# Optimization experiments

Hardware: AMD Instinct MI355X
Metric: run time of the kernel (lower is better)

## Reference

```python
import jax, jax.numpy as jnp
import numpy as np

N, H, F = 131072, 256, 4096
MIN_FRAG = 3
LN_EPS = 1e-5
NORM_EPS = 1e-12
CONSISTENCY_FACTOR = 0.03
INTERMOLECULAR_WEIGHT = 0.2
SCALING_FACTOR = 0.05  # initial_strength at epoch 0 (progressive schedule, eval mode)


def _normalize(x):
    # torch F.normalize(p=2, dim=1): x / max(||x||, eps)
    n = jnp.linalg.norm(x, axis=-1, keepdims=True)
    return x / jnp.maximum(n, NORM_EPS)


def _frag_consistency(feat, frag_ids, valid):
    # size-weighted sum of per-fragment mean deviations == mean deviation over valid atoms
    m = valid.astype(feat.dtype)[:, None]
    seg_sum = jax.ops.segment_sum(feat * m, frag_ids, num_segments=F)
    seg_cnt = jax.ops.segment_sum(m, frag_ids, num_segments=F)
    means = seg_sum / jnp.maximum(seg_cnt, 1.0)  # scatter-mean over valid atoms
    sim = jnp.sum(_normalize(feat) * _normalize(means)[frag_ids], axis=-1)  # [N]
    dev = (1.0 - sim) * valid.astype(feat.dtype)
    return jnp.sum(dev) / jnp.maximum(jnp.sum(valid.astype(feat.dtype)), 1.0)


def setup_inputs() -> dict:
    key = jax.random.key(0)
    ks = jax.random.split(key, 8)
    return {
        "scalar_short": jax.random.normal(ks[0], (N, H), jnp.float32),
        "scalar_long": jax.random.normal(ks[1], (N, H), jnp.float32),
        "vector_short": jax.random.normal(ks[2], (N, 3, H), jnp.float32),
        "vector_long": jax.random.normal(ks[3], (N, 3, H), jnp.float32),
        "fragment_ids": jax.random.randint(ks[4], (N,), 0, F, dtype=jnp.int32),
        "ln_gamma": jnp.ones((H,), jnp.float32),
        "ln_beta": jnp.zeros((H,), jnp.float32),
        "W1": jax.random.normal(ks[5], (H, H), jnp.float32) / np.sqrt(H),
        "b1": jnp.zeros((H,), jnp.float32),
        "Wv": jax.random.normal(ks[6], (H, H), jnp.float32) / np.sqrt(H),
    }


def reference(scalar_short, scalar_long, vector_short, vector_long, fragment_ids,
              ln_gamma, ln_beta, W1, b1, Wv):
    # valid_mask: atoms belonging to fragments of size >= MIN_FRAG
    sizes = jax.ops.segment_sum(jnp.ones((N,), jnp.float32), fragment_ids, num_segments=F)
    valid = sizes[fragment_ids] >= MIN_FRAG  # [N] bool

    # scalar_projector: LayerNorm -> Linear -> SiLU (dropout identity at eval)
    mu = jnp.mean(scalar_short, axis=-1, keepdims=True)
    var = jnp.var(scalar_short, axis=-1, keepdims=True)
    xh = (scalar_short - mu) / jnp.sqrt(var + LN_EPS) * ln_gamma + ln_beta
    scalar_features = jax.nn.silu(xh @ W1.T + b1)  # [N, H]

    intra = _frag_consistency(scalar_features, fragment_ids, valid)

    # vector branch: per-atom magnitude = mean over 3 spatial comps of ||.||_2 over hidden
    vec_mag = jnp.mean(jnp.linalg.norm(vector_short, axis=2), axis=1, keepdims=True)  # [N,1]
    # Linear(bias=False) on mag.expand(-1,H) then [:, :1] == silu(mag * sum(Wv[0,:]))
    w0 = jnp.sum(Wv[0])
    vector_features = jax.nn.silu(vec_mag * w0)  # [N,1]
    vec_loss = _frag_consistency(vector_features, fragment_ids, valid)

    # interfragment differentiation over ALL atoms (no valid mask)
    cnt = jax.ops.segment_sum(jnp.ones((N, 1), jnp.float32), fragment_ids, num_segments=F)
    sfrag = jax.ops.segment_sum(scalar_features, fragment_ids, num_segments=F) / jnp.maximum(cnt, 1.0)
    vfrag = jax.ops.segment_sum(vec_mag, fragment_ids, num_segments=F) / jnp.maximum(cnt, 1.0)
    combined = _normalize(jnp.concatenate([sfrag, vfrag], axis=1))  # [F, H+1]
    sim = combined @ combined.T  # [F, F]
    off_sum = jnp.sum(sim) - jnp.trace(sim)
    inter = off_sum / (F * F - F + 1e-6)

    total = intra + vec_loss + INTERMOLECULAR_WEIGHT * inter
    return CONSISTENCY_FACTOR * total * SCALING_FACTOR
```

## Files before the change

### kernel.cpp

```cpp
#include <hip/hip_runtime.h>
#include <hip/hip_bf16.h>
#include <stdint.h>

#define NA 131072
#define HD 256
#define NF 4096
#define MINFRAG 3
#define LN_EPS 1e-5f
#define NEPS 1e-12f

#define OFF_CNT    0ull
#define OFF_VSUM   16384ull
#define OFF_VFSUM  32768ull
#define OFF_NVSUM  49152ull
#define OFF_FILL   65536ull
#define OFF_DBL    81920ull
#define OFF_SSUM   86016ull
#define OFF_NSUM   4280320ull
#define ZERO_BYTES 8474624ull
#define OFF_OFFS   8474624ull
#define OFF_SVEC   8491008ull
#define OFF_C0     8492032ull
#define OFF_W0     8493056ull
#define OFF_GBF    8493568ull
#define OFF_ORDER  8624640ull

#define IDX_TRACE 257
#define IDX_DEVS  258
#define IDX_DEVV  259
#define IDX_VCNT  260

typedef __attribute__((ext_vector_type(8))) short short8;
typedef __attribute__((ext_vector_type(4))) float f32x4;
union F4S8 { float4 f; short8 s; };
union BFU { __hip_bfloat16 b; unsigned short u; };

__device__ __forceinline__ unsigned short f2b(float x) {
    BFU t; t.b = __float2bfloat16(x); return t.u;
}
__device__ __forceinline__ float b2f(unsigned short u) {
    return __uint_as_float(((uint32_t)u) << 16);
}
__device__ __forceinline__ float silu_f(float x) { return x / (1.f + expf(-x)); }

__global__ __launch_bounds__(256) void k_prep(
    const float* __restrict__ W1, const float* __restrict__ gamma,
    const float* __restrict__ beta, const float* __restrict__ b1,
    const float* __restrict__ Wv,
    unsigned short* __restrict__ Gbf, float* __restrict__ svec,
    float* __restrict__ c0, float* __restrict__ w0) {
    __shared__ float red[8];
    int o = blockIdx.x;
    int t = threadIdx.x;
    if (o < HD) {
        float w = W1[(size_t)o * HD + t];
        unsigned short gb = f2b(w * gamma[t]);
        Gbf[(size_t)o * HD + t] = gb;
        float sp = b2f(gb);
        float cp = w * beta[t];
#pragma unroll
        for (int m = 32; m; m >>= 1) { sp += __shfl_xor(sp, m, 64); cp += __shfl_xor(cp, m, 64); }
        int wv = t >> 6;
        if ((t & 63) == 0) { red[wv] = sp; red[4 + wv] = cp; }
        __syncthreads();
        if (t == 0) {
            svec[o] = red[0] + red[1] + red[2] + red[3];
            c0[o]   = red[4] + red[5] + red[6] + red[7] + b1[o];
        }
    } else {
        float v = Wv[t];
#pragma unroll
        for (int m = 32; m; m >>= 1) v += __shfl_xor(v, m, 64);
        int wv = t >> 6;
        if ((t & 63) == 0) red[wv] = v;
        __syncthreads();
        if (t == 0) w0[0] = red[0] + red[1] + red[2] + red[3];
    }
}

__global__ __launch_bounds__(256) void k_stats(
    const float* __restrict__ vs, const int* __restrict__ fid,
    const float* __restrict__ w0p,
    int* __restrict__ cnt, float* __restrict__ vsum,
    float* __restrict__ vfsum, float* __restrict__ nvsum) {
    int gwave = (blockIdx.x * blockDim.x + threadIdx.x) >> 6;
    int lane = threadIdx.x & 63;
    int nw = (gridDim.x * blockDim.x) >> 6;
    float w0 = w0p[0];
    for (int i = gwave; i < NA; i += nw) {
        const float* base = vs + (size_t)i * 3 * HD;
        float4 v0 = ((const float4*)(base))[lane];
        float4 v1 = ((const float4*)(base + HD))[lane];
        float4 v2 = ((const float4*)(base + 2 * HD))[lane];
        float q0 = v0.x * v0.x + v0.y * v0.y + v0.z * v0.z + v0.w * v0.w;
        float q1 = v1.x * v1.x + v1.y * v1.y + v1.z * v1.z + v1.w * v1.w;
        float q2 = v2.x * v2.x + v2.y * v2.y + v2.z * v2.z + v2.w * v2.w;
#pragma unroll
        for (int m = 32; m; m >>= 1) {
            q0 += __shfl_xor(q0, m, 64);
            q1 += __shfl_xor(q1, m, 64);
            q2 += __shfl_xor(q2, m, 64);
        }
        if (lane == 0) {
            float vm = (sqrtf(q0) + sqrtf(q1) + sqrtf(q2)) * (1.f / 3.f);
            float vf = silu_f(vm * w0);
            float nv = vf / fmaxf(fabsf(vf), NEPS);
            int f = fid[i];
            atomicAdd(&cnt[f], 1);
            atomicAdd(&vsum[f], vm);
            atomicAdd(&vfsum[f], vf);
            atomicAdd(&nvsum[f], nv);
        }
    }
}

__global__ __launch_bounds__(256) void k_scan(const int* __restrict__ cnt,
                                              int* __restrict__ offs) {
    __shared__ int wsum[4];
    int t = threadIdx.x;
    int base = t * 16;
    int c[16];
    int tot = 0;
#pragma unroll
    for (int j = 0; j < 16; ++j) { c[j] = cnt[base + j]; tot += c[j]; }
    int lane = t & 63, w = t >> 6;
    int v = tot;
#pragma unroll
    for (int d = 1; d < 64; d <<= 1) {
        int o = __shfl_up(v, d, 64);
        if (lane >= d) v += o;
    }
    if (lane == 63) wsum[w] = v;
    __syncthreads();
    int wbase = 0;
    for (int i = 0; i < w; ++i) wbase += wsum[i];
    int run = wbase + v - tot;
#pragma unroll
    for (int j = 0; j < 16; ++j) { offs[base + j] = run; run += c[j]; }
}

__global__ __launch_bounds__(256) void k_scatter(
    const int* __restrict__ fid, const int* __restrict__ offs,
    int* __restrict__ fill, int* __restrict__ order) {
    int i = blockIdx.x * blockDim.x + threadIdx.x;
    if (i < NA) {
        int f = fid[i];
        int p = atomicAdd(&fill[f], 1);
        order[offs[f] + p] = i;
    }
}

__global__ __launch_bounds__(256) void k_gemm(
    const float* __restrict__ A, const unsigned short* __restrict__ Gbf,
    const float* __restrict__ svec, const float* __restrict__ c0,
    const int* __restrict__ order, const int* __restrict__ fid,
    const int* __restrict__ offs, const int* __restrict__ cnt,
    float* __restrict__ ssum, float* __restrict__ nsum) {
    __shared__ float4 As16[64 * 8];
    __shared__ float4 Bs16[256 * 8];
    __shared__ float muS[64], rsS[64], rnS[64];
    __shared__ float sqL[64][4];
    __shared__ int fragS[64];

    int tid = threadIdx.x;
    int lane = tid & 63, wid = tid >> 6;
    int r0 = blockIdx.x * 64;
    int rowT = tid >> 4;
    int c4 = tid & 15;

    if (tid < 64) {
        int gi = order[r0 + tid];
        muS[tid] = __int_as_float(gi);
        fragS[tid] = fid[gi];
    }
    __syncthreads();
    int rid[4];
#pragma unroll
    for (int p = 0; p < 4; ++p) rid[p] = __float_as_int(muS[16 * p + rowT]);
    __syncthreads();

    f32x4 acc[4][4] = {};
    float s1p[4] = {0, 0, 0, 0}, s2p[4] = {0, 0, 0, 0};

    for (int k0 = 0; k0 < HD; k0 += 64) {
#pragma unroll
        for (int p = 0; p < 4; ++p) {
            int row = 16 * p + rowT;
            float4 v = *(const float4*)(A + (size_t)rid[p] * HD + k0 + c4 * 4);
            s1p[p] += v.x + v.y + v.z + v.w;
            s2p[p] += v.x * v.x + v.y * v.y + v.z * v.z + v.w * v.w;
            ushort4 pk;
            pk.x = f2b(v.x); pk.y = f2b(v.y); pk.z = f2b(v.z); pk.w = f2b(v.w);
            int slot = row * 8 + ((c4 >> 1) ^ (row & 7));
            ((ushort4*)&As16[slot])[c4 & 1] = pk;
        }
#pragma unroll
        for (int p = 0; p < 8; ++p) {
            int u = p * 256 + tid;
            int n = u >> 3, cc = u & 7;
            float4 g = *(const float4*)(Gbf + (size_t)n * HD + k0 + cc * 8);
            Bs16[n * 8 + (cc ^ (n & 7))] = g;
        }
        __syncthreads();
#pragma unroll
        for (int kk = 0; kk < 2; ++kk) {
            int uo = kk * 4 + (lane >> 4);
            short8 a[4], b[4];
#pragma unroll
            for (int mi = 0; mi < 4; ++mi) {
                int r = mi * 16 + (lane & 15);
                F4S8 t_; t_.f = As16[r * 8 + (uo ^ (r & 7))];
                a[mi] = t_.s;
            }
#pragma unroll
            for (int ni = 0; ni < 4; ++ni) {
                int n = wid * 64 + ni * 16 + (lane & 15);
                F4S8 t_; t_.f = Bs16[n * 8 + (uo ^ (n & 7))];
                b[ni] = t_.s;
            }
#pragma unroll
            for (int mi = 0; mi < 4; ++mi)
#pragma unroll
                for (int ni = 0; ni < 4; ++ni)
                    acc[mi][ni] = __builtin_amdgcn_mfma_f32_16x16x32_bf16(
                        a[mi], b[ni], acc[mi][ni], 0, 0, 0);
        }
        __syncthreads();
    }
#pragma unroll
    for (int p = 0; p < 4; ++p) {
        float s1 = s1p[p], s2 = s2p[p];
#pragma unroll
        for (int m = 1; m < 16; m <<= 1) {
            s1 += __shfl_xor(s1, m, 64);
            s2 += __shfl_xor(s2, m, 64);
        }
        if (c4 == 0) {
            int row = 16 * p + rowT;
            float mu_ = s1 * (1.f / HD);
            float var = s2 * (1.f / HD) - mu_ * mu_;
            muS[row] = mu_;
            rsS[row] = rsqrtf(var + LN_EPS);
        }
    }
    __syncthreads();
    float sv[4], cv[4];
#pragma unroll
    for (int ni = 0; ni < 4; ++ni) {
        int c = wid * 64 + ni * 16 + (lane & 15);
        sv[ni] = svec[c];
        cv[ni] = c0[c];
    }
    unsigned short* featS = (unsigned short*)Bs16;
    float sq[4][4];
#pragma unroll
    for (int mi = 0; mi < 4; ++mi)
#pragma unroll
        for (int q = 0; q < 4; ++q) {
            int rl = mi * 16 + (lane >> 4) * 4 + q;
            float mu_ = muS[rl], rs_ = rsS[rl];
            float sqa = 0.f;
#pragma unroll
            for (int ni = 0; ni < 4; ++ni) {
                int c = wid * 64 + ni * 16 + (lane & 15);
                float pre = rs_ * (acc[mi][ni][q] - mu_ * sv[ni]) + cv[ni];
                unsigned short us = f2b(silu_f(pre));
                featS[rl * 256 + (c ^ ((rl & 7) << 2))] = us;
                float fr = b2f(us);
                sqa += fr * fr;
            }
            sq[mi][q] = sqa;
        }
#pragma unroll
    for (int mi = 0; mi < 4; ++mi)
#pragma unroll
        for (int q = 0; q < 4; ++q) {
            float s_ = sq[mi][q];
            s_ += __shfl_xor(s_, 1, 64);
            s_ += __shfl_xor(s_, 2, 64);
            s_ += __shfl_xor(s_, 4, 64);
            s_ += __shfl_xor(s_, 8, 64);
            if ((lane & 15) == 0) sqL[mi * 16 + (lane >> 4) * 4 + q][wid] = s_;
        }
    __syncthreads();
    if (tid < 64) {
        float t = sqL[tid][0] + sqL[tid][1] + sqL[tid][2] + sqL[tid][3];
        rnS[tid] = 1.f / fmaxf(sqrtf(t), NEPS);
    }
    __syncthreads();
    int cc = wid * 64 + lane;
    float sAcc = 0.f, nAcc = 0.f;
    int curF = fragS[0];
    for (int row = 0; row < 64; ++row) {
        int f = fragS[row];
        if (f != curF) {
            int gs = offs[curF], n = cnt[curF];
            if (gs >= r0 && gs + n <= r0 + 64) {
                ssum[(size_t)curF * HD + cc] = sAcc;
                nsum[(size_t)curF * HD + cc] = nAcc;
            } else {
                atomicAdd(&ssum[(size_t)curF * HD + cc], sAcc);
                atomicAdd(&nsum[(size_t)curF * HD + cc], nAcc);
            }
            sAcc = 0.f; nAcc = 0.f; curF = f;
        }
        float v = b2f(featS[row * 256 + (cc ^ ((row & 7) << 2))]);
        sAcc += v;
        nAcc = fmaf(v, rnS[row], nAcc);
    }
    {
        int gs = offs[curF], n = cnt[curF];
        if (gs >= r0 && gs + n <= r0 + 64) {
            ssum[(size_t)curF * HD + cc] = sAcc;
            nsum[(size_t)curF * HD + cc] = nAcc;
        } else {
            atomicAdd(&ssum[(size_t)curF * HD + cc], sAcc);
            atomicAdd(&nsum[(size_t)curF * HD + cc], nAcc);
        }
    }
}

__global__ __launch_bounds__(256) void k_frag(
    const float* __restrict__ ssum, const float* __restrict__ nsum,
    const int* __restrict__ cnt, const float* __restrict__ vsum,
    const float* __restrict__ vfsum, const float* __restrict__ nvsum,
    double* __restrict__ dbl) {
    int gwave = (blockIdx.x * blockDim.x + threadIdx.x) >> 6;
    int lane = threadIdx.x & 63;
    int nw = (gridDim.x * blockDim.x) >> 6;

    double la0 = 0, la1 = 0, la2 = 0, la3 = 0;
    double lv = 0, ltr = 0, lvc = 0, ldS = 0, ldV = 0;

    for (int f = gwave; f < NF; f += nw) {
        float4 s = ((const float4*)(ssum + (size_t)f * HD))[lane];
        float4 nn = ((const float4*)(nsum + (size_t)f * HD))[lane];
        int c = cnt[f];
        float ssq = s.x * s.x + s.y * s.y + s.z * s.z + s.w * s.w;
        float dsn = nn.x * s.x + nn.y * s.y + nn.z * s.z + nn.w * s.w;
#pragma unroll
        for (int m = 32; m; m >>= 1) {
            ssq += __shfl_xor(ssq, m, 64);
            dsn += __shfl_xor(dsn, m, 64);
        }
        float inv_all = 1.f / fmaxf((float)c, 1.f);
        float m0 = s.x * inv_all, m1 = s.y * inv_all, m2 = s.z * inv_all, m3 = s.w * inv_all;
        float ssq_mean = ssq * inv_all * inv_all;
        float vfr = vsum[f] * inv_all;
        float nrm2 = ssq_mean + vfr * vfr;
        float inv = 1.f / fmaxf(sqrtf(nrm2), NEPS);
        la0 += (double)(m0 * inv);
        la1 += (double)(m1 * inv);
        la2 += (double)(m2 * inv);
        la3 += (double)(m3 * inv);
        if (lane == 0) {
            lv += (double)(vfr * inv);
            ltr += (double)(nrm2 * inv * inv);
            if (c >= MINFRAG) {
                lvc += (double)c;
                float denom = fmaxf(sqrtf(ssq), NEPS);
                ldS += (double)c - (double)(dsn / denom);
                float vfm = vfsum[f] * inv_all;
                float vsgn = vfm / fmaxf(fabsf(vfm), NEPS);
                ldV += (double)c - (double)(vsgn * nvsum[f]);
            }
        }
    }
    atomicAdd(&dbl[4 * lane + 0], la0);
    atomicAdd(&dbl[4 * lane + 1], la1);
    atomicAdd(&dbl[4 * lane + 2], la2);
    atomicAdd(&dbl[4 * lane + 3], la3);
    if (lane == 0) {
        atomicAdd(&dbl[256], lv);
        atomicAdd(&dbl[IDX_TRACE], ltr);
        atomicAdd(&dbl[IDX_VCNT], lvc);
        atomicAdd(&dbl[IDX_DEVS], ldS);
        atomicAdd(&dbl[IDX_DEVV], ldV);
    }
}

__global__ __launch_bounds__(64) void k_final(const double* __restrict__ dbl,
                                              float* __restrict__ out) {
    if (threadIdx.x == 0 && blockIdx.x == 0) {
        double s2 = 0;
        for (int d = 0; d < 257; ++d) s2 += dbl[d] * dbl[d];
        double off = s2 - dbl[IDX_TRACE];
        double inter = off / ((double)NF * NF - NF + 1e-6);
        double vc = fmax(dbl[IDX_VCNT], 1.0);
        double total = dbl[IDX_DEVS] / vc + dbl[IDX_DEVV] / vc + 0.2 * inter;
        out[0] = (float)(0.03 * 0.05 * total);
    }
}

extern "C" void kernel_launch(void* const* d_in, const int* in_sizes, int n_in,
                              void* d_out, int out_size, void* d_ws, size_t ws_size,
                              hipStream_t stream) {
    const float* scalar_short = (const float*)d_in[0];
    const float* vector_short = (const float*)d_in[2];
    const int* fragment_ids = (const int*)d_in[4];
    const float* ln_gamma = (const float*)d_in[5];
    const float* ln_beta = (const float*)d_in[6];
    const float* W1 = (const float*)d_in[7];
    const float* b1 = (const float*)d_in[8];
    const float* Wv = (const float*)d_in[9];
    float* out = (float*)d_out;

    char* ws = (char*)d_ws;
    int* cnt = (int*)(ws + OFF_CNT);
    float* vsum = (float*)(ws + OFF_VSUM);
    float* vfsum = (float*)(ws + OFF_VFSUM);
    float* nvsum = (float*)(ws + OFF_NVSUM);
    int* fill = (int*)(ws + OFF_FILL);
    double* dbl = (double*)(ws + OFF_DBL);
    float* ssum = (float*)(ws + OFF_SSUM);
    float* nsum = (float*)(ws + OFF_NSUM);
    int* offs = (int*)(ws + OFF_OFFS);
    float* svec = (float*)(ws + OFF_SVEC);
    float* c0 = (float*)(ws + OFF_C0);
    float* w0 = (float*)(ws + OFF_W0);
    unsigned short* Gbf = (unsigned short*)(ws + OFF_GBF);
    int* order = (int*)(ws + OFF_ORDER);

    hipMemsetAsync(ws, 0, ZERO_BYTES, stream);
    k_prep<<<HD + 1, 256, 0, stream>>>(W1, ln_gamma, ln_beta, b1, Wv, Gbf, svec, c0, w0);
    k_stats<<<2048, 256, 0, stream>>>(vector_short, fragment_ids, w0, cnt, vsum, vfsum, nvsum);
    k_scan<<<1, 256, 0, stream>>>(cnt, offs);
    k_scatter<<<NA / 256, 256, 0, stream>>>(fragment_ids, offs, fill, order);
    k_gemm<<<NA / 64, 256, 0, stream>>>(scalar_short, Gbf, svec, c0, order,
                                        fragment_ids, offs, cnt, ssum, nsum);
    k_frag<<<64, 256, 0, stream>>>(ssum, nsum, cnt, vsum, vfsum, nvsum, dbl);
    k_final<<<1, 64, 0, stream>>>(dbl, out);
}
```

Measured before the change: 252.7 us.

## Restructure gemm to load B fragments from global, unroll stats, custom zero kernel

The GEMM kernel now stages the whole 64x256 A tile in LDS once and reads the bf16 weight fragments straight from global/L2 into registers, dropping the per-K-step B staging in shared memory and its barriers. The stats kernel handles two atoms per wave per iteration to get more loads in flight. hipMemsetAsync is replaced by a custom float4 zeroing kernel, and SiLU uses the fast exp with a hardware reciprocal. The trade-offs are more global/L2 traffic for the weights (each wave re-reads them) and slightly lower SiLU precision, in exchange for fewer barriers and less LDS use, which may allow higher occupancy.

```diff
diff --git a/kernel.cpp b/kernel.cpp
--- a/kernel.cpp
+++ b/kernel.cpp
@@ -41,7 +41,15 @@
 __device__ __forceinline__ float b2f(unsigned short u) {
     return __uint_as_float(((uint32_t)u) << 16);
 }
-__device__ __forceinline__ float silu_f(float x) { return x / (1.f + expf(-x)); }
+__device__ __forceinline__ float silu_f(float x) {
+    return x * __builtin_amdgcn_rcpf(1.f + __expf(-x));
+}
+
+__global__ __launch_bounds__(256) void k_zero(float4* __restrict__ z) {
+    int i = blockIdx.x * 256 + threadIdx.x;
+    float4 v = {0.f, 0.f, 0.f, 0.f};
+    z[i] = v;
+}
 
 __global__ __launch_bounds__(256) void k_prep(
     const float* __restrict__ W1, const float* __restrict__ gamma,
@@ -87,29 +95,46 @@
     int lane = threadIdx.x & 63;
     int nw = (gridDim.x * blockDim.x) >> 6;
     float w0 = w0p[0];
-    for (int i = gwave; i < NA; i += nw) {
-        const float* base = vs + (size_t)i * 3 * HD;
-        float4 v0 = ((const float4*)(base))[lane];
-        float4 v1 = ((const float4*)(base + HD))[lane];
-        float4 v2 = ((const float4*)(base + 2 * HD))[lane];
-        float q0 = v0.x * v0.x + v0.y * v0.y + v0.z * v0.z + v0.w * v0.w;
-        float q1 = v1.x * v1.x + v1.y * v1.y + v1.z * v1.z + v1.w * v1.w;
-        float q2 = v2.x * v2.x + v2.y * v2.y + v2.z * v2.z + v2.w * v2.w;
+    for (int i0 = gwave * 2; i0 < NA; i0 += nw * 2) {
+        const float* ba = vs + (size_t)i0 * 3 * HD;
+        const float* bb = vs + (size_t)(i0 + 1) * 3 * HD;
+        float4 a0 = ((const float4*)(ba))[lane];
+        float4 a1 = ((const float4*)(ba + HD))[lane];
+        float4 a2 = ((const float4*)(ba + 2 * HD))[lane];
+        float4 b0 = ((const float4*)(bb))[lane];
+        float4 b1 = ((const float4*)(bb + HD))[lane];
+        float4 b2 = ((const float4*)(bb + 2 * HD))[lane];
+        float qa0 = a0.x * a0.x + a0.y * a0.y + a0.z * a0.z + a0.w * a0.w;
+        float qa1 = a1.x * a1.x + a1.y * a1.y + a1.z * a1.z + a1.w * a1.w;
+        float qa2 = a2.x * a2.x + a2.y * a2.y + a2.z * a2.z + a2.w * a2.w;
+        float qb0 = b0.x * b0.x + b0.y * b0.y + b0.z * b0.z + b0.w * b0.w;
+        float qb1 = b1.x * b1.x + b1.y * b1.y + b1.z * b1.z + b1.w * b1.w;
+        float qb2 = b2.x * b2.x + b2.y * b2.y + b2.z * b2.z + b2.w * b2.w;
 #pragma unroll
         for (int m = 32; m; m >>= 1) {
-            q0 += __shfl_xor(q0, m, 64);
-            q1 += __shfl_xor(q1, m, 64);
-            q2 += __shfl_xor(q2, m, 64);
+            qa0 += __shfl_xor(qa0, m, 64);
+            qa1 += __shfl_xor(qa1, m, 64);
+            qa2 += __shfl_xor(qa2, m, 64);
+            qb0 += __shfl_xor(qb0, m, 64);
+            qb1 += __shfl_xor(qb1, m, 64);
+            qb2 += __shfl_xor(qb2, m, 64);
         }
         if (lane == 0) {
-            float vm = (sqrtf(q0) + sqrtf(q1) + sqrtf(q2)) * (1.f / 3.f);
-            float vf = silu_f(vm * w0);
-            float nv = vf / fmaxf(fabsf(vf), NEPS);
-            int f = fid[i];
-            atomicAdd(&cnt[f], 1);
-            atomicAdd(&vsum[f], vm);
-            atomicAdd(&vfsum[f], vf);
-            atomicAdd(&nvsum[f], nv);
+            float vma = (sqrtf(qa0) + sqrtf(qa1) + sqrtf(qa2)) * (1.f / 3.f);
+            float vmb = (sqrtf(qb0) + sqrtf(qb1) + sqrtf(qb2)) * (1.f / 3.f);
+            float vfa = silu_f(vma * w0);
+            float vfb = silu_f(vmb * w0);
+            float nva = vfa / fmaxf(fabsf(vfa), NEPS);
+            float nvb = vfb / fmaxf(fabsf(vfb), NEPS);
+            int fa = fid[i0], fb = fid[i0 + 1];
+            atomicAdd(&cnt[fa], 1);
+            atomicAdd(&vsum[fa], vma);
+            atomicAdd(&vfsum[fa], vfa);
+            atomicAdd(&nvsum[fa], nva);
+            atomicAdd(&cnt[fb], 1);
+            atomicAdd(&vsum[fb], vmb);
+            atomicAdd(&vfsum[fb], vfb);
+            atomicAdd(&nvsum[fb], nvb);
         }
     }
 }
@@ -156,11 +181,10 @@
     const int* __restrict__ order, const int* __restrict__ fid,
     const int* __restrict__ offs, const int* __restrict__ cnt,
     float* __restrict__ ssum, float* __restrict__ nsum) {
-    __shared__ float4 As16[64 * 8];
-    __shared__ float4 Bs16[256 * 8];
+    __shared__ float4 As16[64 * 32];
     __shared__ float muS[64], rsS[64], rnS[64];
     __shared__ float sqL[64][4];
-    __shared__ int fragS[64];
+    __shared__ int ridS[64], fragS[64];
 
     int tid = threadIdx.x;
     int lane = tid & 63, wid = tid >> 6;
@@ -170,63 +194,28 @@
 
     if (tid < 64) {
         int gi = order[r0 + tid];
-        muS[tid] = __int_as_float(gi);
+        ridS[tid] = gi;
         fragS[tid] = fid[gi];
     }
     __syncthreads();
     int rid[4];
 #pragma unroll
-    for (int p = 0; p < 4; ++p) rid[p] = __float_as_int(muS[16 * p + rowT]);
-    __syncthreads();
-
-    f32x4 acc[4][4] = {};
+    for (int p = 0; p < 4; ++p) rid[p] = ridS[16 * p + rowT];
+
     float s1p[4] = {0, 0, 0, 0}, s2p[4] = {0, 0, 0, 0};
-
-    for (int k0 = 0; k0 < HD; k0 += 64) {
+#pragma unroll
+    for (int kc = 0; kc < 4; ++kc)
 #pragma unroll
         for (int p = 0; p < 4; ++p) {
             int row = 16 * p + rowT;
-            float4 v = *(const float4*)(A + (size_t)rid[p] * HD + k0 + c4 * 4);
+            float4 v = *(const float4*)(A + (size_t)rid[p] * HD + kc * 64 + c4 * 4);
             s1p[p] += v.x + v.y + v.z + v.w;
             s2p[p] += v.x * v.x + v.y * v.y + v.z * v.z + v.w * v.w;
             ushort4 pk;
             pk.x = f2b(v.x); pk.y = f2b(v.y); pk.z = f2b(v.z); pk.w = f2b(v.w);
-            int slot = row * 8 + ((c4 >> 1) ^ (row & 7));
+            int slot = row * 32 + kc * 8 + ((c4 >> 1) ^ (row & 7));
             ((ushort4*)&As16[slot])[c4 & 1] = pk;
         }
-#pragma unroll
-        for (int p = 0; p < 8; ++p) {
-            int u = p * 256 + tid;
-            int n = u >> 3, cc = u & 7;
-            float4 g = *(const float4*)(Gbf + (size_t)n * HD + k0 + cc * 8);
-            Bs16[n * 8 + (cc ^ (n & 7))] = g;
-        }
-        __syncthreads();
-#pragma unroll
-        for (int kk = 0; kk < 2; ++kk) {
-            int uo = kk * 4 + (lane >> 4);
-            short8 a[4], b[4];
-#pragma unroll
-            for (int mi = 0; mi < 4; ++mi) {
-                int r = mi * 16 + (lane & 15);
-                F4S8 t_; t_.f = As16[r * 8 + (uo ^ (r & 7))];
-                a[mi] = t_.s;
-            }
-#pragma unroll
-            for (int ni = 0; ni < 4; ++ni) {
-                int n = wid * 64 + ni * 16 + (lane & 15);
-                F4S8 t_; t_.f = Bs16[n * 8 + (uo ^ (n & 7))];
-                b[ni] = t_.s;
-            }
-#pragma unroll
-            for (int mi = 0; mi < 4; ++mi)
-#pragma unroll
-                for (int ni = 0; ni < 4; ++ni)
-                    acc[mi][ni] = __builtin_amdgcn_mfma_f32_16x16x32_bf16(
-                        a[mi], b[ni], acc[mi][ni], 0, 0, 0);
-        }
-        __syncthreads();
-    }
 #pragma unroll
     for (int p = 0; p < 4; ++p) {
         float s1 = s1p[p], s2 = s2p[p];
@@ -244,6 +233,42 @@
         }
     }
     __syncthreads();
+
+    int lg = lane >> 4;
+    const unsigned short* bp[4];
+#pragma unroll
+    for (int ni = 0; ni < 4; ++ni)
+        bp[ni] = Gbf + (size_t)(wid * 64 + ni * 16 + (lane & 15)) * HD + lg * 8;
+
+    f32x4 acc[4][4] = {};
+#pragma unroll
+    for (int kc = 0; kc < 4; ++kc) {
+        short8 bfr[2][4];
+#pragma unroll
+        for (int kk = 0; kk < 2; ++kk)
+#pragma unroll
+            for (int ni = 0; ni < 4; ++ni)
+                bfr[kk][ni] = *(const short8*)(bp[ni] + kc * 64 + kk * 32);
+#pragma unroll
+        for (int kk = 0; kk < 2; ++kk) {
+            int jp = kk * 4 + lg;
+            short8 a[4];
+#pragma unroll
+            for (int mi = 0; mi < 4; ++mi) {
+                int r = mi * 16 + (lane & 15);
+                F4S8 t_; t_.f = As16[r * 32 + kc * 8 + (jp ^ (r & 7))];
+                a[mi] = t_.s;
+            }
+#pragma unroll
+            for (int mi = 0; mi < 4; ++mi)
+#pragma unroll
+                for (int ni = 0; ni < 4; ++ni)
+                    acc[mi][ni] = __builtin_amdgcn_mfma_f32_16x16x32_bf16(
+                        a[mi], bfr[kk][ni], acc[mi][ni], 0, 0, 0);
+        }
+    }
+    __syncthreads();
+
     float sv[4], cv[4];
 #pragma unroll
     for (int ni = 0; ni < 4; ++ni) {
@@ -251,7 +276,7 @@
         sv[ni] = svec[c];
         cv[ni] = c0[c];
     }
-    unsigned short* featS = (unsigned short*)Bs16;
+    unsigned short* featS = (unsigned short*)As16;
     float sq[4][4];
 #pragma unroll
     for (int mi = 0; mi < 4; ++mi)
@@ -421,7 +446,7 @@
     unsigned short* Gbf = (unsigned short*)(ws + OFF_GBF);
     int* order = (int*)(ws + OFF_ORDER);
 
-    hipMemsetAsync(ws, 0, ZERO_BYTES, stream);
+    k_zero<<<2069, 256, 0, stream>>>((float4*)ws);
     k_prep<<<HD + 1, 256, 0, stream>>>(W1, ln_gamma, ln_beta, b1, Wv, Gbf, svec, c0, w0);
     k_stats<<<2048, 256, 0, stream>>>(vector_short, fragment_ids, w0, cnt, vsum, vfsum, nvsum);
     k_scan<<<1, 256, 0, stream>>>(cnt, offs);
```

Result: no change. 250.7 us (-0.8%).
